# Kernel optimization log

Hardware: AMD Instinct MI355X
Metric: run time of the kernel (lower is better)

Reference implementation:

```python
import jax, jax.numpy as jnp
import numpy as np

H, D_MODEL, D_K, D_V = 16, 1024, 64, 64
B, L = 2, 2048


def setup_inputs() -> dict:
    key = jax.random.key(0)
    ks = jax.random.split(key, 9)
    s = 1.0 / np.sqrt(D_MODEL)
    return {
        "Q": jax.random.normal(ks[0], (B, L, D_MODEL), jnp.float32),
        "K": jax.random.normal(ks[1], (B, L, D_MODEL), jnp.float32),
        "V": jax.random.normal(ks[2], (B, L, D_MODEL), jnp.float32),
        "mask": jax.random.randint(ks[3], (B, L), 0, 2, jnp.int32),
        "W_Q": jax.random.uniform(ks[4], (D_MODEL, H * D_K), jnp.float32, -s, s),
        "b_Q": jax.random.uniform(ks[5], (H * D_K,), jnp.float32, -s, s),
        "W_K": jax.random.uniform(ks[6], (D_MODEL, H * D_K), jnp.float32, -s, s),
        "W_V": jax.random.uniform(ks[7], (D_MODEL, H * D_V), jnp.float32, -s, s),
        "b_V": jax.random.uniform(ks[8], (H * D_V,), jnp.float32, -s, s),
    }


def reference(Q, K, V, mask, W_Q, b_Q, W_K, W_V, b_V):
    b, lq, _ = Q.shape
    lk = K.shape[1]
    scale = jnp.sqrt(jnp.float32(D_K))
    # projections -> [b, h, len, d]
    q = (Q @ W_Q + b_Q).reshape(b, lq, H, D_K).transpose(0, 2, 1, 3)
    k = (K @ W_K).reshape(b, lk, H, D_K).transpose(0, 2, 1, 3)
    v = (V @ W_V + b_V).reshape(b, lk, H, D_V).transpose(0, 2, 1, 3)
    # scores [b*h, lq, lk]
    A = jnp.einsum("bhqd,bhkd->bhqk", q, k).reshape(b * H, lq, lk) / scale
    # faithful to torch: mask.repeat(h, len_k).view(b*h, -1, len_k)
    mask_rep = jnp.tile(mask, (H, lk)).reshape(b * H, -1, lk)
    A = jnp.where(mask_rep == 0, jnp.float32(-1e9), A)
    alpha = jax.nn.softmax(A, axis=2)
    out = jnp.einsum("bhqk,bhkd->bhqd", alpha.reshape(b, H, lq, lk), v)
    return out.transpose(0, 2, 1, 3).reshape(b, lq, H * D_V)
```

## Files before the change

kernel.cpp:

```cpp
#include <hip/hip_runtime.h>
#include <hip/hip_bf16.h>

typedef float f32x4 __attribute__((ext_vector_type(4)));
typedef short s16x4 __attribute__((ext_vector_type(4)));
typedef unsigned int u32;
typedef unsigned short u16;
typedef unsigned int u32x2 __attribute__((ext_vector_type(2)));
typedef unsigned int u32x4 __attribute__((ext_vector_type(4)));
typedef unsigned short u16x4 __attribute__((ext_vector_type(4)));
typedef unsigned short u16x8 __attribute__((ext_vector_type(8)));

#define MFMA16(a, b, c) __builtin_amdgcn_mfma_f32_16x16x16bf16_1k((a), (b), (c), 0, 0, 0)

#define QSCALE 0.18033688f

__device__ __forceinline__ void mfma32(f32x4& acc, u16x8 a, u16x8 b) {
  asm("v_mfma_f32_16x16x32_bf16 %0, %1, %2, %0" : "+v"(acc) : "v"(a), "v"(b));
}

__device__ __forceinline__ void gload16(const u16* g, u16* l) {
  __builtin_amdgcn_global_load_lds((const __attribute__((address_space(1))) void*)g,
                                   (__attribute__((address_space(3))) void*)l, 16, 0, 0);
}

__device__ __forceinline__ u16 f2bf(float f) {
  u32 u = __builtin_bit_cast(u32, f);
  u += 0x7fffu + ((u >> 16) & 1u);
  return (u16)(u >> 16);
}

__device__ __forceinline__ u32 pk2(float lo, float hi) {
  u32 d;
  asm("v_cvt_pk_bf16_f32 %0, %1, %2" : "=v"(d) : "v"(lo), "v"(hi));
  return d;
}

__device__ __forceinline__ float ex2(float x) {
  float r;
  asm("v_exp_f32 %0, %1" : "=v"(r) : "v"(x));
  return r;
}

__global__ __launch_bounds__(256) void convX(const float* __restrict__ Q, const float* __restrict__ K,
                                             const float* __restrict__ V, u16* __restrict__ o) {
  const int z = blockIdx.y;
  const float* s = z == 0 ? Q : (z == 1 ? K : V);
  const size_t i = ((size_t)blockIdx.x * 256 + threadIdx.x) * 4;
  float4 v4 = *(const float4*)&s[i];
  u16x4 ob = { f2bf(v4.x), f2bf(v4.y), f2bf(v4.z), f2bf(v4.w) };
  *(u16x4*)&o[(size_t)z * 4194304 + i] = ob;
}

__global__ __launch_bounds__(256) void convW(const float* __restrict__ WQ, const float* __restrict__ WK,
                                             const float* __restrict__ WV, u16* __restrict__ o) {
  const int z = blockIdx.z;
  const float* W = z == 0 ? WQ : (z == 1 ? WK : WV);
  const int k0 = blockIdx.x * 8, n = blockIdx.y * 256 + threadIdx.x;
  u16x8 ob;
  #pragma unroll
  for (int j = 0; j < 8; ++j) ob[j] = f2bf(W[(size_t)(k0 + j) * 1024 + n]);
  *(u16x8*)&o[(size_t)z * 1048576 + (size_t)n * 1024 + k0] = ob;
}

__global__ __launch_bounds__(256) void proj_fast(
    const u16* __restrict__ Xb, const u16* __restrict__ Wt,
    const float* __restrict__ bQ, const float* __restrict__ bV, u16* __restrict__ Y0) {
  const int z = blockIdx.z;
  const u16* X = Xb + (size_t)z * 4194304;
  const u16* W = Wt + (size_t)z * 1048576;
  u16* Y = Y0 + (size_t)z * 4194304;
  const float* bias = (z == 0) ? bQ : (z == 1) ? nullptr : bV;
  const float scale = (z == 0) ? QSCALE : 1.0f;

  __shared__ u16 Alds[128][64];
  __shared__ u16 Blds[128][64];

  const int tid = threadIdx.x;
  const int w = tid >> 6, ln = tid & 63, g = ln >> 4, q16 = ln & 15;
  const int x7 = q16 & 7;
  const int wr = w >> 1, wc = w & 1;
  const int rowbase = blockIdx.y * 128, cbase = blockIdx.x * 128;

  const int srow = w * 8 + (ln >> 3);
  const int sch = (ln & 7) ^ ((ln >> 3) & 7);
  const u16* Xg = X + (size_t)(rowbase + srow) * 1024 + sch * 8;
  const u16* Wg = W + (size_t)(cbase + srow) * 1024 + sch * 8;
  u16* Abase = &Alds[0][0] + w * 512;
  u16* Bbase = &Blds[0][0] + w * 512;

  f32x4 acc[4][4] = {};

  for (int k0 = 0; k0 < 1024; k0 += 64) {
    #pragma unroll
    for (int p = 0; p < 4; ++p) {
      gload16(Xg + (size_t)p * 32768 + k0, Abase + p * 2048);
      gload16(Wg + (size_t)p * 32768 + k0, Bbase + p * 2048);
    }
    __syncthreads();

    u16x8 af[4][2], bfr[4][2];
    #pragma unroll
    for (int mi = 0; mi < 4; ++mi)
      #pragma unroll
      for (int ks = 0; ks < 2; ++ks)
        af[mi][ks] = *(const u16x8*)&Alds[wr * 64 + mi * 16 + q16][((ks * 4 + g) ^ x7) * 8];
    #pragma unroll
    for (int ni = 0; ni < 4; ++ni)
      #pragma unroll
      for (int ks = 0; ks < 2; ++ks)
        bfr[ni][ks] = *(const u16x8*)&Blds[wc * 64 + ni * 16 + q16][((ks * 4 + g) ^ x7) * 8];

    #pragma unroll
    for (int mi = 0; mi < 4; ++mi)
      #pragma unroll
      for (int ni = 0; ni < 4; ++ni) {
        mfma32(acc[mi][ni], af[mi][0], bfr[ni][0]);
        mfma32(acc[mi][ni], af[mi][1], bfr[ni][1]);
      }
    __syncthreads();
  }

  #pragma unroll
  for (int ni = 0; ni < 4; ++ni) {
    const int c = cbase + wc * 64 + ni * 16 + q16;
    const float bi = bias ? bias[c] : 0.0f;
    const int hh = c >> 6, d = c & 63;
    #pragma unroll
    for (int mi = 0; mi < 4; ++mi)
      #pragma unroll
      for (int r = 0; r < 4; ++r) {
        const int grow = rowbase + wr * 64 + mi * 16 + g * 4 + r;
        const int bb = grow >> 11, l = grow & 2047;
        const float val = (acc[mi][ni][r] + bi) * scale;
        const size_t idx = (z == 2)
            ? (((size_t)(bb * 16 + hh)) * 64 + d) * 2048 + l
            : (((size_t)(bb * 16 + hh)) * 2048 + l) * 64 + d;
        Y[idx] = f2bf(val);
      }
  }
}

__global__ __launch_bounds__(256) void proj_legacy(
    const float* __restrict__ Qin, const float* __restrict__ Kin, const float* __restrict__ Vin,
    const float* __restrict__ WQ, const float* __restrict__ WK, const float* __restrict__ WV,
    const float* __restrict__ bQ, const float* __restrict__ bV,
    u16* __restrict__ ws) {
  const int z = blockIdx.z;
  const float* X = (z == 0) ? Qin : (z == 1) ? Kin : Vin;
  const float* W = (z == 0) ? WQ : (z == 1) ? WK : WV;
  const float* bias = (z == 0) ? bQ : (z == 1) ? nullptr : bV;
  u16* Y = ws + (size_t)z * 4194304;
  const float scale = (z == 0) ? QSCALE : 1.0f;

  __shared__ u16 Alds[128][40];
  __shared__ u16 Blds[128][40];

  const int tid = threadIdx.x;
  const int w = tid >> 6, ln = tid & 63, g = ln >> 4, q16 = ln & 15;
  const int wr = w >> 1, wc = w & 1;
  const int rowbase = blockIdx.y * 128, cbase = blockIdx.x * 128;

  f32x4 acc[4][4] = {};

  for (int k0 = 0; k0 < 1024; k0 += 32) {
    #pragma unroll
    for (int i = 0; i < 4; ++i) {
      int idx = tid + i * 256;
      int row = idx >> 3, kq = idx & 7;
      const float4 a = *(const float4*)&X[(size_t)(rowbase + row) * 1024 + k0 + kq * 4];
      u16x4 pk = { f2bf(a.x), f2bf(a.y), f2bf(a.z), f2bf(a.w) };
      *(u16x4*)&Alds[row][kq * 4] = pk;
    }
    #pragma unroll
    for (int i = 0; i < 4; ++i) {
      int idx = tid + i * 256;
      int kk = idx >> 5, nq = idx & 31;
      const float4 wv = *(const float4*)&W[(size_t)(k0 + kk) * 1024 + cbase + nq * 4];
      Blds[nq * 4 + 0][kk] = f2bf(wv.x);
      Blds[nq * 4 + 1][kk] = f2bf(wv.y);
      Blds[nq * 4 + 2][kk] = f2bf(wv.z);
      Blds[nq * 4 + 3][kk] = f2bf(wv.w);
    }
    __syncthreads();

    s16x4 af[4][2], bfr[4][2];
    #pragma unroll
    for (int mi = 0; mi < 4; ++mi)
      #pragma unroll
      for (int s = 0; s < 2; ++s)
        af[mi][s] = *(const s16x4*)&Alds[wr * 64 + mi * 16 + q16][s * 16 + g * 4];
    #pragma unroll
    for (int ni = 0; ni < 4; ++ni)
      #pragma unroll
      for (int s = 0; s < 2; ++s)
        bfr[ni][s] = *(const s16x4*)&Blds[wc * 64 + ni * 16 + q16][s * 16 + g * 4];

    #pragma unroll
    for (int mi = 0; mi < 4; ++mi)
      #pragma unroll
      for (int ni = 0; ni < 4; ++ni) {
        acc[mi][ni] = MFMA16(af[mi][0], bfr[ni][0], acc[mi][ni]);
        acc[mi][ni] = MFMA16(af[mi][1], bfr[ni][1], acc[mi][ni]);
      }
    __syncthreads();
  }

  #pragma unroll
  for (int ni = 0; ni < 4; ++ni) {
    const int c = cbase + wc * 64 + ni * 16 + q16;
    const float bi = bias ? bias[c] : 0.0f;
    const int hh = c >> 6, d = c & 63;
    #pragma unroll
    for (int mi = 0; mi < 4; ++mi)
      #pragma unroll
      for (int r = 0; r < 4; ++r) {
        const int grow = rowbase + wr * 64 + mi * 16 + g * 4 + r;
        const int bb = grow >> 11, l = grow & 2047;
        const float val = (acc[mi][ni][r] + bi) * scale;
        const size_t idx = (z == 2)
            ? (((size_t)(bb * 16 + hh)) * 64 + d) * 2048 + l
            : (((size_t)(bb * 16 + hh)) * 2048 + l) * 64 + d;
        Y[idx] = f2bf(val);
      }
  }
}

__global__ __launch_bounds__(256) void attn_kernel(
    const u16* __restrict__ ws, const int* __restrict__ mask,
    float* __restrict__ out, float* __restrict__ part1, float* __restrict__ pl) {
  __shared__ u16 klds[4096];
  __shared__ u16 vtlds[4096];
  __shared__ u16 pt[4][16][72];

  const int bh = blockIdx.y, b = bh >> 4, h = bh & 15;
  const int qbase = blockIdx.x * 64;
  const int half = blockIdx.z;
  const int koff = half << 10;
  float* po = half ? part1 : out;
  float* plh = pl + half * 65536;

  const u16* qp = ws + (size_t)bh * 131072;
  const u16* kp = ws + 4194304 + (size_t)bh * 131072;
  const u16* vp = ws + 8388608 + (size_t)bh * 131072;
  const int* maskrow = mask + (h & 1) * 2048;

  const int tid = threadIdx.x;
  const int w = tid >> 6, ln = tid & 63, g = ln >> 4, q16 = ln & 15;
  const int x7 = q16 & 7;
  const int qrow = qbase + w * 16 + q16;

  u16x8 qf0 = *(const u16x8*)(qp + (size_t)qrow * 64 + g * 8);
  u16x8 qf1 = *(const u16x8*)(qp + (size_t)qrow * 64 + 32 + g * 8);

  const int srow = w * 8 + (ln >> 3);
  const int sch = (ln & 7) ^ (ln >> 3);
  const u16* kg = kp + (size_t)srow * 64 + sch * 8;
  const u16* vg = vp + (size_t)srow * 2048 + sch * 8;

  float l_ = 0.f;
  f32x4 ov[4] = {};

  for (int kt = koff; kt < koff + 1024; kt += 64) {
    __syncthreads();
    gload16(kg + (size_t)kt * 64, klds + w * 512);
    gload16(kg + (size_t)kt * 64 + 2048, klds + w * 512 + 2048);
    gload16(vg + kt, vtlds + w * 512);
    gload16(vg + kt + 65536, vtlds + w * 512 + 2048);
    const unsigned long long bal = __ballot(maskrow[kt + ln] != 0);
    __syncthreads();

    f32x4 sf[4];
    #pragma unroll
    for (int f = 0; f < 4; ++f) {
      u16x8 kf0 = *(const u16x8*)&klds[(f * 16 + q16) * 64 + (g ^ x7) * 8];
      u16x8 kf1 = *(const u16x8*)&klds[(f * 16 + q16) * 64 + ((4 + g) ^ x7) * 8];
      f32x4 s = { 0.f, 0.f, 0.f, 0.f };
      mfma32(s, kf0, qf0);
      mfma32(s, kf1, qf1);
      sf[f] = s;
    }
    {
      const u32 blo = (u32)bal, bhi = (u32)(bal >> 32);
      #pragma unroll
      for (int f = 0; f < 4; ++f) {
        const u32 nib = (((f & 2) ? bhi : blo) >> (16 * (f & 1) + 4 * g)) & 15u;
        #pragma unroll
        for (int r2 = 0; r2 < 4; ++r2)
          if (!((nib >> r2) & 1u)) sf[f][r2] = -1e9f;
      }
    }

    #pragma unroll
    for (int f = 0; f < 4; ++f)
      #pragma unroll
      for (int r2 = 0; r2 < 4; ++r2)
        sf[f][r2] = ex2(sf[f][r2]);
    l_ += ((sf[0][0] + sf[0][1]) + (sf[0][2] + sf[0][3])) +
          ((sf[1][0] + sf[1][1]) + (sf[1][2] + sf[1][3])) +
          ((sf[2][0] + sf[2][1]) + (sf[2][2] + sf[2][3])) +
          ((sf[3][0] + sf[3][1]) + (sf[3][2] + sf[3][3]));

    #pragma unroll
    for (int f = 0; f < 4; ++f) {
      u32x2 pw = { pk2(sf[f][0], sf[f][1]), pk2(sf[f][2], sf[f][3]) };
      *(u16x4*)&pt[w][q16][f * 16 + 4 * g] = __builtin_bit_cast(u16x4, pw);
    }
    asm volatile("s_waitcnt lgkmcnt(0)" ::: "memory");
    u16x8 pa0 = *(const u16x8*)&pt[w][q16][g * 8];
    u16x8 pa1 = *(const u16x8*)&pt[w][q16][32 + g * 8];
    asm volatile("" ::: "memory");

    #pragma unroll
    for (int dc = 0; dc < 4; ++dc) {
      u16x8 vf0 = *(const u16x8*)&vtlds[(dc * 16 + q16) * 64 + (g ^ x7) * 8];
      u16x8 vf1 = *(const u16x8*)&vtlds[(dc * 16 + q16) * 64 + ((4 + g) ^ x7) * 8];
      mfma32(ov[dc], vf0, pa0);
      mfma32(ov[dc], vf1, pa1);
    }
  }

  l_ += __shfl_xor(l_, 16);
  l_ += __shfl_xor(l_, 32);
  if ((ln & 48) == 0) plh[bh * 2048 + qrow] = l_;
  #pragma unroll
  for (int dc = 0; dc < 4; ++dc) {
    float4 o4 = { ov[dc][0], ov[dc][1], ov[dc][2], ov[dc][3] };
    *(float4*)&po[((size_t)(b * 2048 + qbase + w * 16 + q16)) * 1024 + h * 64 + dc * 16 + 4 * g] = o4;
  }
}

__global__ __launch_bounds__(256) void combine_kernel(
    float* __restrict__ out, const float* __restrict__ part1, const float* __restrict__ pl) {
  const int e = blockIdx.x * 256 + threadIdx.x;
  const int i = e * 4;
  const int b = i >> 21;
  const int rem = i & 2097151;
  const int q = rem >> 10;
  const int c = rem & 1023;
  const int h = c >> 6;
  const int bhq = ((b * 16 + h) << 11) + q;
  const float rinv = 1.0f / (pl[bhq] + pl[65536 + bhq]);
  float4 a = *(const float4*)&out[i];
  float4 p = *(const float4*)&part1[i];
  float4 r = { (a.x + p.x) * rinv, (a.y + p.y) * rinv, (a.z + p.z) * rinv, (a.w + p.w) * rinv };
  *(float4*)&out[i] = r;
}

extern "C" void kernel_launch(void* const* d_in, const int* in_sizes, int n_in,
                              void* d_out, int out_size, void* d_ws, size_t ws_size,
                              hipStream_t stream) {
  const float* Qin = (const float*)d_in[0];
  const float* Kin = (const float*)d_in[1];
  const float* Vin = (const float*)d_in[2];
  const int* mask = (const int*)d_in[3];
  const float* WQ = (const float*)d_in[4];
  const float* bQ = (const float*)d_in[5];
  const float* WK = (const float*)d_in[6];
  const float* WV = (const float*)d_in[7];
  const float* bV = (const float*)d_in[8];
  float* out = (float*)d_out;
  u16* ws = (u16*)d_ws;

  float* part1 = (float*)(ws + 12582912);
  float* pl = (float*)(ws + 12582912 + 8388608);

  const bool fast = ws_size >= (size_t)56623104;
  if (fast) {
    convX<<<dim3(4096, 3), 256, 0, stream>>>(Qin, Kin, Vin, ws + 12582912);
    convW<<<dim3(128, 4, 3), 256, 0, stream>>>(WQ, WK, WV, ws + 25165824);
    proj_fast<<<dim3(8, 32, 3), 256, 0, stream>>>(ws + 12582912, ws + 25165824, bQ, bV, ws);
  } else {
    proj_legacy<<<dim3(8, 32, 3), 256, 0, stream>>>(Qin, Kin, Vin, WQ, WK, WV, bQ, bV, ws);
  }
  attn_kernel<<<dim3(32, 32, 2), 256, 0, stream>>>(ws, mask, out, part1, pl);
  combine_kernel<<<4096, 256, 0, stream>>>(out, part1, pl);
}
```

Baseline: 133.9 us.

## Process two 16-row query tiles per wave to reuse K/V LDS fragments

Each wave now handles 32 query rows instead of 16, so each block covers 128 queries and the grid's x dimension is halved. Every K and V fragment read from LDS, along with each block's global-to-LDS loads of K/V tiles, now serves two MFMA tiles, halving K/V traffic per query. The cost is more registers per thread, more LDS for the P staging buffer, and half as many blocks (1024), which could lower occupancy and latency hiding on a GPU with many CUs.

```diff
diff --git a/kernel.cpp b/kernel.cpp
--- a/kernel.cpp
+++ b/kernel.cpp
@@ -230,10 +230,10 @@
     float* __restrict__ out, float* __restrict__ part1, float* __restrict__ pl) {
   __shared__ u16 klds[4096];
   __shared__ u16 vtlds[4096];
-  __shared__ u16 pt[4][16][72];
+  __shared__ u16 pt[4][2][16][72];
 
   const int bh = blockIdx.y, b = bh >> 4, h = bh & 15;
-  const int qbase = blockIdx.x * 64;
+  const int qbase = blockIdx.x * 128;
   const int half = blockIdx.z;
   const int koff = half << 10;
   float* po = half ? part1 : out;
@@ -247,18 +247,21 @@
   const int tid = threadIdx.x;
   const int w = tid >> 6, ln = tid & 63, g = ln >> 4, q16 = ln & 15;
   const int x7 = q16 & 7;
-  const int qrow = qbase + w * 16 + q16;
-
-  u16x8 qf0 = *(const u16x8*)(qp + (size_t)qrow * 64 + g * 8);
-  u16x8 qf1 = *(const u16x8*)(qp + (size_t)qrow * 64 + 32 + g * 8);
+
+  u16x8 qf[2][2];
+  #pragma unroll
+  for (int u = 0; u < 2; ++u)
+    #pragma unroll
+    for (int s = 0; s < 2; ++s)
+      qf[u][s] = *(const u16x8*)(qp + (size_t)(qbase + w * 32 + u * 16 + q16) * 64 + s * 32 + g * 8);
 
   const int srow = w * 8 + (ln >> 3);
   const int sch = (ln & 7) ^ (ln >> 3);
   const u16* kg = kp + (size_t)srow * 64 + sch * 8;
   const u16* vg = vp + (size_t)srow * 2048 + sch * 8;
 
-  float l_ = 0.f;
-  f32x4 ov[4] = {};
+  float l_[2] = { 0.f, 0.f };
+  f32x4 ov[2][4] = {};
 
   for (int kt = koff; kt < koff + 1024; kt += 64) {
     __syncthreads();
@@ -269,15 +272,18 @@
     const unsigned long long bal = __ballot(maskrow[kt + ln] != 0);
     __syncthreads();
 
-    f32x4 sf[4];
+    f32x4 sf[2][4];
     #pragma unroll
     for (int f = 0; f < 4; ++f) {
       u16x8 kf0 = *(const u16x8*)&klds[(f * 16 + q16) * 64 + (g ^ x7) * 8];
       u16x8 kf1 = *(const u16x8*)&klds[(f * 16 + q16) * 64 + ((4 + g) ^ x7) * 8];
-      f32x4 s = { 0.f, 0.f, 0.f, 0.f };
-      mfma32(s, kf0, qf0);
-      mfma32(s, kf1, qf1);
-      sf[f] = s;
+      #pragma unroll
+      for (int u = 0; u < 2; ++u) {
+        f32x4 s = { 0.f, 0.f, 0.f, 0.f };
+        mfma32(s, kf0, qf[u][0]);
+        mfma32(s, kf1, qf[u][1]);
+        sf[u][f] = s;
+      }
     }
     {
       const u32 blo = (u32)bal, bhi = (u32)(bal >> 32);
@@ -286,46 +292,60 @@
         const u32 nib = (((f & 2) ? bhi : blo) >> (16 * (f & 1) + 4 * g)) & 15u;
         #pragma unroll
         for (int r2 = 0; r2 < 4; ++r2)
-          if (!((nib >> r2) & 1u)) sf[f][r2] = -1e9f;
-      }
-    }
-
-    #pragma unroll
-    for (int f = 0; f < 4; ++f)
-      #pragma unroll
-      for (int r2 = 0; r2 < 4; ++r2)
-        sf[f][r2] = ex2(sf[f][r2]);
-    l_ += ((sf[0][0] + sf[0][1]) + (sf[0][2] + sf[0][3])) +
-          ((sf[1][0] + sf[1][1]) + (sf[1][2] + sf[1][3])) +
-          ((sf[2][0] + sf[2][1]) + (sf[2][2] + sf[2][3])) +
-          ((sf[3][0] + sf[3][1]) + (sf[3][2] + sf[3][3]));
-
-    #pragma unroll
-    for (int f = 0; f < 4; ++f) {
-      u32x2 pw = { pk2(sf[f][0], sf[f][1]), pk2(sf[f][2], sf[f][3]) };
-      *(u16x4*)&pt[w][q16][f * 16 + 4 * g] = __builtin_bit_cast(u16x4, pw);
+          if (!((nib >> r2) & 1u)) { sf[0][f][r2] = -1e9f; sf[1][f][r2] = -1e9f; }
+      }
+    }
+
+    #pragma unroll
+    for (int u = 0; u < 2; ++u) {
+      #pragma unroll
+      for (int f = 0; f < 4; ++f)
+        #pragma unroll
+        for (int r2 = 0; r2 < 4; ++r2)
+          sf[u][f][r2] = ex2(sf[u][f][r2]);
+      l_[u] += ((sf[u][0][0] + sf[u][0][1]) + (sf[u][0][2] + sf[u][0][3])) +
+               ((sf[u][1][0] + sf[u][1][1]) + (sf[u][1][2] + sf[u][1][3])) +
+               ((sf[u][2][0] + sf[u][2][1]) + (sf[u][2][2] + sf[u][2][3])) +
+               ((sf[u][3][0] + sf[u][3][1]) + (sf[u][3][2] + sf[u][3][3]));
+
+      #pragma unroll
+      for (int f = 0; f < 4; ++f) {
+        u32x2 pw = { pk2(sf[u][f][0], sf[u][f][1]), pk2(sf[u][f][2], sf[u][f][3]) };
+        *(u16x4*)&pt[w][u][q16][f * 16 + 4 * g] = __builtin_bit_cast(u16x4, pw);
+      }
     }
     asm volatile("s_waitcnt lgkmcnt(0)" ::: "memory");
-    u16x8 pa0 = *(const u16x8*)&pt[w][q16][g * 8];
-    u16x8 pa1 = *(const u16x8*)&pt[w][q16][32 + g * 8];
+    u16x8 pa0[2], pa1[2];
+    #pragma unroll
+    for (int u = 0; u < 2; ++u) {
+      pa0[u] = *(const u16x8*)&pt[w][u][q16][g * 8];
+      pa1[u] = *(const u16x8*)&pt[w][u][q16][32 + g * 8];
+    }
     asm volatile("" ::: "memory");
 
     #pragma unroll
     for (int dc = 0; dc < 4; ++dc) {
       u16x8 vf0 = *(const u16x8*)&vtlds[(dc * 16 + q16) * 64 + (g ^ x7) * 8];
       u16x8 vf1 = *(const u16x8*)&vtlds[(dc * 16 + q16) * 64 + ((4 + g) ^ x7) * 8];
-      mfma32(ov[dc], vf0, pa0);
-      mfma32(ov[dc], vf1, pa1);
-    }
-  }
-
-  l_ += __shfl_xor(l_, 16);
-  l_ += __shfl_xor(l_, 32);
-  if ((ln & 48) == 0) plh[bh * 2048 + qrow] = l_;
-  #pragma unroll
-  for (int dc = 0; dc < 4; ++dc) {
-    float4 o4 = { ov[dc][0], ov[dc][1], ov[dc][2], ov[dc][3] };
-    *(float4*)&po[((size_t)(b * 2048 + qbase + w * 16 + q16)) * 1024 + h * 64 + dc * 16 + 4 * g] = o4;
+      #pragma unroll
+      for (int u = 0; u < 2; ++u) {
+        mfma32(ov[u][dc], vf0, pa0[u]);
+        mfma32(ov[u][dc], vf1, pa1[u]);
+      }
+    }
+  }
+
+  #pragma unroll
+  for (int u = 0; u < 2; ++u) {
+    l_[u] += __shfl_xor(l_[u], 16);
+    l_[u] += __shfl_xor(l_[u], 32);
+    const int qrow = qbase + w * 32 + u * 16 + q16;
+    if ((ln & 48) == 0) plh[bh * 2048 + qrow] = l_[u];
+    #pragma unroll
+    for (int dc = 0; dc < 4; ++dc) {
+      float4 o4 = { ov[u][dc][0], ov[u][dc][1], ov[u][dc][2], ov[u][dc][3] };
+      *(float4*)&po[((size_t)(b * 2048 + qrow)) * 1024 + h * 64 + dc * 16 + 4 * g] = o4;
+    }
   }
 }
 
@@ -372,6 +392,6 @@
   } else {
     proj_legacy<<<dim3(8, 32, 3), 256, 0, stream>>>(Qin, Kin, Vin, WQ, WK, WV, bQ, bV, ws);
   }
-  attn_kernel<<<dim3(32, 32, 2), 256, 0, stream>>>(ws, mask, out, part1, pl);
+  attn_kernel<<<dim3(16, 32, 2), 256, 0, stream>>>(ws, mask, out, part1, pl);
   combine_kernel<<<4096, 256, 0, stream>>>(out, part1, pl);
 }
```

Result: faster. 125.8 us (-6.1%).
